# Kernel optimization log

Hardware: AMD Instinct MI355X
Metric: run time of the kernel (lower is better)

The kernel has to match this reference:

```python
import jax, jax.numpy as jnp
import numpy as np

N_NODES = 100000
N_EDGES = 800000
D = 128
N_GRAPHS = 512


def _graph_conv(h, src, dst, norm_src, norm_dst, W, b):
    # DGL GraphConv, norm='both': h' = relu(D_in^{-1/2} * sum_{(u->v)} (D_out^{-1/2} h_u) W + b)
    m = (h * norm_src[:, None])[src]                      # [E, d] gather
    agg = jax.ops.segment_sum(m, dst, num_segments=N_NODES)  # [N, d] scatter-add
    return jax.nn.relu(agg * norm_dst[:, None] @ W + b)


def setup_inputs() -> dict:
    key = jax.random.key(0)
    ks = jax.random.split(key, 10)
    src = jax.random.randint(ks[0], (N_EDGES,), 0, N_NODES)
    dst = jax.random.randint(ks[1], (N_EDGES,), 0, N_NODES)
    graph_ids = jnp.sort(jax.random.randint(ks[2], (N_ODES := N_NODES,), 0, N_GRAPHS))
    features = jax.random.normal(ks[3], (N_NODES, D), dtype=jnp.float32)
    s = 1.0 / np.sqrt(D)
    w1 = jax.random.uniform(ks[4], (D, D), jnp.float32, -s, s)
    b1 = jnp.zeros((D,), jnp.float32)
    w2 = jax.random.uniform(ks[5], (D, D), jnp.float32, -s, s)
    b2 = jnp.zeros((D,), jnp.float32)
    wg = jax.random.uniform(ks[6], (D, 1), jnp.float32, -s, s)
    bg = jnp.zeros((1,), jnp.float32)
    return {"src": src, "dst": dst, "graph_ids": graph_ids, "features": features,
            "w1": w1, "b1": b1, "w2": w2, "b2": b2, "wg": wg, "bg": bg}


def reference(src, dst, graph_ids, features, w1, b1, w2, b2, wg, bg):
    ones = jnp.ones((N_EDGES,), jnp.float32)
    deg_out = jax.ops.segment_sum(ones, src, num_segments=N_NODES)
    deg_in = jax.ops.segment_sum(ones, dst, num_segments=N_NODES)
    norm_src = jax.lax.rsqrt(jnp.maximum(deg_out, 1.0))
    norm_dst = jax.lax.rsqrt(jnp.maximum(deg_in, 1.0))

    h = _graph_conv(features, src, dst, norm_src, norm_dst, w1, b1)
    # dropout is identity in eval mode
    h = _graph_conv(h, src, dst, norm_src, norm_dst, w2, b2)

    # weighted graph aggregation: sigmoid gate per node, per-graph weighted sum
    gate = jax.nn.sigmoid(h @ wg + bg)                    # [N, 1]
    wh = jax.ops.segment_sum(gate * h, graph_ids, num_segments=N_GRAPHS)  # [G, d]
    return wh, h
```

## Files before the change

kernel.cpp:

```cpp
#include <hip/hip_runtime.h>

#define D 128
#define G_GRAPHS 512
#define CCHUNK 4
#define NSLICE 64
#define BINMAX 25088

typedef _Float16 f16;
typedef _Float16 f16x2 __attribute__((ext_vector_type(2)));
typedef _Float16 f16x4 __attribute__((ext_vector_type(4)));
typedef _Float16 f16x8 __attribute__((ext_vector_type(8)));
typedef float f32x2 __attribute__((ext_vector_type(2)));
typedef float f32x4 __attribute__((ext_vector_type(4)));
typedef unsigned short u16;
typedef unsigned char u8;

#define SCAN_CHUNK 2048

__global__ __launch_bounds__(256) void hist_kernel(const int* __restrict__ src, const int* __restrict__ dst,
                                                   u8* __restrict__ pho, u8* __restrict__ phi,
                                                   u8* __restrict__ rank,
                                                   int E, int N, int slice_len, int binsz) {
    __shared__ unsigned hp[(BINMAX + 3) / 4];
    int c = blockIdx.x, role = blockIdx.y, s = blockIdx.z;
    int c0 = c * binsz;
    int lim = min(binsz, N - c0);
    int nw = (lim + 3) >> 2;
    for (int i = threadIdx.x; i < nw; i += 256) hp[i] = 0;
    __syncthreads();
    const int* arr = role ? dst : src;
    int e1 = min(E, (s + 1) * slice_len);
    if (role) {
        for (int e = s * slice_len + (int)threadIdx.x; e < e1; e += 256) {
            unsigned v = (unsigned)(arr[e] - c0);
            if (v < (unsigned)lim) {
                int sh = (v & 3) * 8;
                unsigned old = atomicAdd(&hp[v >> 2], 1u << sh);
                rank[e] = (u8)((old >> sh) & 0xffu);
            }
        }
    } else {
        for (int e = s * slice_len + (int)threadIdx.x; e < e1; e += 256) {
            unsigned v = (unsigned)(arr[e] - c0);
            if (v < (unsigned)lim)
                atomicAdd(&hp[v >> 2], 1u << ((v & 3) * 8));
        }
    }
    __syncthreads();
    u8* outp = (role ? phi : pho) + (size_t)s * N + c0;
    int nw4 = lim >> 2;
    unsigned* o32 = (unsigned*)outp;
    for (int i = threadIdx.x; i < nw4; i += 256) o32[i] = hp[i];
    for (int i = nw4 * 4 + (int)threadIdx.x; i < lim; i += 256)
        outp[i] = (u8)((hp[i >> 2] >> ((i & 3) * 8)) & 0xffu);
}

__global__ __launch_bounds__(256) void merge_prescale_kernel(const u8* __restrict__ pho, u8* __restrict__ phi,
                                                             const float* __restrict__ feat,
                                                             float* __restrict__ norm_src, float* __restrict__ norm_dst,
                                                             int* __restrict__ deg_in_total,
                                                             unsigned* __restrict__ X1,
                                                             const int* __restrict__ gid, int* __restrict__ gstart,
                                                             int mb, int N, int G) {
    if ((int)blockIdx.x >= mb) {
        int n = ((int)blockIdx.x - mb) * 256 + (int)threadIdx.x;
        if (n >= N) return;
        int g = gid[n];
        if (n == 0) {
            for (int x = 0; x <= g; ++x) gstart[x] = 0;
        } else {
            int pg = gid[n - 1];
            for (int x = pg + 1; x <= g; ++x) gstart[x] = n;
        }
        if (n == N - 1) {
            for (int x = g + 1; x <= G; ++x) gstart[x] = N;
        }
        return;
    }
    __shared__ int sumo[4][64];
    __shared__ int sumi[4][64];
    __shared__ float ns_l[64];
    int nl = threadIdx.x & 63;
    int sg = threadIdx.x >> 6;
    int nbase = blockIdx.x * 64;
    int n = nbase + nl;
    int ph_vals[16];
    int po = 0, pp = 0;
    if (n < N) {
        #pragma unroll
        for (int j = 0; j < 16; ++j) {
            int s = sg * 16 + j;
            po += pho[(size_t)s * N + n];
            int v = phi[(size_t)s * N + n];
            ph_vals[j] = v;
            pp += v;
        }
    }
    sumo[sg][nl] = po;
    sumi[sg][nl] = pp;
    __syncthreads();
    if (n < N) {
        int base_i = 0;
        #pragma unroll
        for (int g = 0; g < 4; ++g) base_i += (g < sg) ? sumi[g][nl] : 0;
        int run = base_i;
        #pragma unroll
        for (int j = 0; j < 16; ++j) {
            int s = sg * 16 + j;
            phi[(size_t)s * N + n] = (u8)run;
            run += ph_vals[j];
        }
        if (sg == 0) {
            int tot_o = sumo[0][nl] + sumo[1][nl] + sumo[2][nl] + sumo[3][nl];
            int tot_i = sumi[0][nl] + sumi[1][nl] + sumi[2][nl] + sumi[3][nl];
            float nsv = rsqrtf(fmaxf((float)tot_o, 1.0f));
            norm_src[n] = nsv;
            ns_l[nl] = nsv;
            deg_in_total[n] = tot_i;
            norm_dst[n] = rsqrtf(fmaxf((float)tot_i, 1.0f));
        }
    }
    __syncthreads();
    int cnt = (min(64, N - nbase)) * 32;
    const float4* f4 = (const float4*)feat + (size_t)nbase * 32;
    unsigned* o4 = X1 + (size_t)nbase * 32;
    for (int k = threadIdx.x; k < cnt; k += 256) {
        float4 v = f4[k];
        float s = ns_l[k >> 5];
        int pk = __builtin_amdgcn_cvt_pk_fp8_f32(v.x * s, v.y * s, 0, false);
        pk = __builtin_amdgcn_cvt_pk_fp8_f32(v.z * s, v.w * s, pk, true);
        o4[k] = (unsigned)pk;
    }
}

__global__ __launch_bounds__(256) void scan1_kernel(const int* __restrict__ deg,
                                                    int* __restrict__ partial,
                                                    int* __restrict__ blocksums, int n) {
    __shared__ int wsum[4];
    int lane = threadIdx.x & 63, wid = threadIdx.x >> 6;
    int base = blockIdx.x * SCAN_CHUNK + (int)threadIdx.x * 8;
    int v[8]; int tsum = 0;
    #pragma unroll
    for (int i = 0; i < 8; ++i) { v[i] = (base + i < n) ? deg[base + i] : 0; tsum += v[i]; }
    int s = tsum;
    #pragma unroll
    for (int off = 1; off < 64; off <<= 1) {
        int t = __shfl_up(s, off);
        if (lane >= off) s += t;
    }
    if (lane == 63) wsum[wid] = s;
    __syncthreads();
    int woff = 0;
    for (int w = 0; w < wid; ++w) woff += wsum[w];
    int run = woff + s - tsum;
    #pragma unroll
    for (int i = 0; i < 8; ++i) {
        if (base + i < n) partial[base + i] = run;
        run += v[i];
        if (base + i == n - 1) partial[n] = run;
    }
    if (threadIdx.x == 255) blocksums[blockIdx.x] = woff + s;
}

__global__ void scan2_kernel(int* __restrict__ bs, int nb) {
    int lane = threadIdx.x;
    int carry = 0;
    for (int base = 0; base < nb; base += 64) {
        int i = base + lane;
        int v = (i < nb) ? bs[i] : 0;
        int s = v;
        #pragma unroll
        for (int off = 1; off < 64; off <<= 1) {
            int t = __shfl_up(s, off);
            if (lane >= off) s += t;
        }
        if (i < nb) bs[i] = carry + s - v;
        carry += __shfl(s, 63);
    }
}

__global__ __launch_bounds__(256) void fill_kernel(const int* __restrict__ src, const int* __restrict__ dst,
                                                   const int* __restrict__ partial, const int* __restrict__ bs,
                                                   const u8* __restrict__ phi, const u8* __restrict__ rank,
                                                   int* __restrict__ csr_src,
                                                   int E, int N, int slice_len) {
    int s = blockIdx.y;
    int e = s * slice_len + blockIdx.x * 256 + threadIdx.x;
    int e1 = min(E, (s + 1) * slice_len);
    if (e >= e1) return;
    int d = dst[e];
    int p = partial[d] + bs[d >> 11] + (int)phi[(size_t)s * N + d] + (int)rank[e];
    csr_src[p] = src[e];
}

#define GATHER_BLOCKS 2048
__global__ __launch_bounds__(256) void gather_kernel(const unsigned* __restrict__ x,
                                                     const float* __restrict__ norm_dst,
                                                     const int* __restrict__ partial, const int* __restrict__ bs,
                                                     const int* __restrict__ csr_src,
                                                     f16* __restrict__ A, int N) {
    int wid0 = blockIdx.x * 4 + ((int)threadIdx.x >> 6);
    int lane = threadIdx.x & 63;
    int g = lane >> 4;
    int l = lane & 15;
    for (int node0 = wid0; node0 < N; node0 += GATHER_BLOCKS * 4) {
        int node = __builtin_amdgcn_readfirstlane(node0);
        int beg = partial[node] + bs[node >> 11];
        int end = partial[node + 1] + bs[(node + 1) >> 11];
        float acc0[8] = {0.f}, acc1[8] = {0.f};
        int e = beg;
        for (; e + 8 <= end; e += 8) {
            int sa = csr_src[e + g];
            int sb = csr_src[e + 4 + g];
            uint2 wa = *(const uint2*)(x + (size_t)sa * 32 + l * 2);
            uint2 wb = *(const uint2*)(x + (size_t)sb * 32 + l * 2);
            f32x2 p0 = __builtin_amdgcn_cvt_pk_f32_fp8((int)wa.x, false);
            f32x2 p1 = __builtin_amdgcn_cvt_pk_f32_fp8((int)wa.x, true);
            f32x2 p2 = __builtin_amdgcn_cvt_pk_f32_fp8((int)wa.y, false);
            f32x2 p3 = __builtin_amdgcn_cvt_pk_f32_fp8((int)wa.y, true);
            acc0[0] += p0.x; acc0[1] += p0.y; acc0[2] += p1.x; acc0[3] += p1.y;
            acc0[4] += p2.x; acc0[5] += p2.y; acc0[6] += p3.x; acc0[7] += p3.y;
            f32x2 q0 = __builtin_amdgcn_cvt_pk_f32_fp8((int)wb.x, false);
            f32x2 q1 = __builtin_amdgcn_cvt_pk_f32_fp8((int)wb.x, true);
            f32x2 q2 = __builtin_amdgcn_cvt_pk_f32_fp8((int)wb.y, false);
            f32x2 q3 = __builtin_amdgcn_cvt_pk_f32_fp8((int)wb.y, true);
            acc1[0] += q0.x; acc1[1] += q0.y; acc1[2] += q1.x; acc1[3] += q1.y;
            acc1[4] += q2.x; acc1[5] += q2.y; acc1[6] += q3.x; acc1[7] += q3.y;
        }
        if (e + 4 <= end) {
            int sa = csr_src[e + g];
            uint2 wa = *(const uint2*)(x + (size_t)sa * 32 + l * 2);
            f32x2 p0 = __builtin_amdgcn_cvt_pk_f32_fp8((int)wa.x, false);
            f32x2 p1 = __builtin_amdgcn_cvt_pk_f32_fp8((int)wa.x, true);
            f32x2 p2 = __builtin_amdgcn_cvt_pk_f32_fp8((int)wa.y, false);
            f32x2 p3 = __builtin_amdgcn_cvt_pk_f32_fp8((int)wa.y, true);
            acc0[0] += p0.x; acc0[1] += p0.y; acc0[2] += p1.x; acc0[3] += p1.y;
            acc0[4] += p2.x; acc0[5] += p2.y; acc0[6] += p3.x; acc0[7] += p3.y;
            e += 4;
        }
        int rem = end - e;
        if (g < rem) {
            int sa = csr_src[e + g];
            uint2 wa = *(const uint2*)(x + (size_t)sa * 32 + l * 2);
            f32x2 p0 = __builtin_amdgcn_cvt_pk_f32_fp8((int)wa.x, false);
            f32x2 p1 = __builtin_amdgcn_cvt_pk_f32_fp8((int)wa.x, true);
            f32x2 p2 = __builtin_amdgcn_cvt_pk_f32_fp8((int)wa.y, false);
            f32x2 p3 = __builtin_amdgcn_cvt_pk_f32_fp8((int)wa.y, true);
            acc1[0] += p0.x; acc1[1] += p0.y; acc1[2] += p1.x; acc1[3] += p1.y;
            acc1[4] += p2.x; acc1[5] += p2.y; acc1[6] += p3.x; acc1[7] += p3.y;
        }
        float nd = norm_dst[node];
        f16x8 o;
        #pragma unroll
        for (int j = 0; j < 8; ++j) {
            float v = acc0[j] + acc1[j];
            v += __shfl_xor(v, 16);
            v += __shfl_xor(v, 32);
            o[j] = (f16)(v * nd);
        }
        if (g == 0) *(f16x8*)(A + (size_t)node * D + l * 8) = o;
    }
}

template <typename OutT, bool FP8OUT, bool SCALE, bool GATE>
__global__ __launch_bounds__(256) void gemm_kernel(const f16* __restrict__ A,
                                                   const float* __restrict__ Wg,
                                                   const float* __restrict__ bias,
                                                   const float* __restrict__ rowscale,
                                                   const float* __restrict__ wgv,
                                                   const float* __restrict__ bgv,
                                                   float* __restrict__ gate_out,
                                                   OutT* __restrict__ out, int M) {
    __shared__ f16 Wf[4 * 8 * 64 * 8];
    for (int i = threadIdx.x; i < 2048; i += 256) {
        int kg = i >> 7, j = i & 127;
        int k0 = kg * 8;
        f16x8 tmp;
        #pragma unroll
        for (int b = 0; b < 8; ++b) tmp[b] = (f16)Wg[(k0 + b) * D + j];
        int t = k0 >> 5, c = j >> 4;
        int l = ((k0 & 31) >> 3) * 16 + (j & 15);
        *(f16x8*)&Wf[((t * 8 + c) * 64 + l) * 8] = tmp;
    }
    __syncthreads();
    int wave = threadIdx.x >> 6, lane = threadIdx.x & 63;

    for (int row0 = (blockIdx.x * 4 + wave) * 16; row0 < M; row0 += gridDim.x * 64) {
        int arow = row0 + (lane & 15);
        const f16* Abase = A + arow * D + (lane >> 4) * 8;
        f16x8 a[4];
        #pragma unroll
        for (int t = 0; t < 4; ++t) a[t] = *(const f16x8*)(Abase + t * 32);

        float ns[4];
        if (SCALE) {
            #pragma unroll
            for (int r = 0; r < 4; ++r) ns[r] = rowscale[row0 + (lane >> 4) * 4 + r];
        }
        float dotr[4] = {0.f, 0.f, 0.f, 0.f};

        #pragma unroll
        for (int c = 0; c < 8; ++c) {
            f32x4 acc = {0.f, 0.f, 0.f, 0.f};
            #pragma unroll
            for (int t = 0; t < 4; ++t) {
                f16x8 bf = *(const f16x8*)&Wf[((t * 8 + c) * 64 + lane) * 8];
                acc = __builtin_amdgcn_mfma_f32_16x16x32_f16(a[t], bf, acc, 0, 0, 0);
            }
            int col = c * 16 + (lane & 15);
            float bj = bias[col];
            float wgc = GATE ? wgv[col] : 0.f;
            #pragma unroll
            for (int r = 0; r < 4; ++r) {
                int row = row0 + (lane >> 4) * 4 + r;
                float v = fmaxf(acc[r] + bj, 0.f);
                if (SCALE) v *= ns[r];
                if (FP8OUT) {
                    int pk = __builtin_amdgcn_cvt_pk_fp8_f32(v, v, 0, false);
                    ((u8*)out)[(size_t)row * D + col] = (u8)(pk & 0xff);
                } else {
                    out[(size_t)row * D + col] = (OutT)v;
                }
                if (GATE) dotr[r] += v * wgc;
            }
        }
        if (GATE) {
            float bg0 = bgv[0];
            #pragma unroll
            for (int r = 0; r < 4; ++r) {
                float d = dotr[r];
                d += __shfl_xor(d, 1); d += __shfl_xor(d, 2);
                d += __shfl_xor(d, 4); d += __shfl_xor(d, 8);
                if ((lane & 15) == 0)
                    gate_out[row0 + (lane >> 4) * 4 + r] = 1.0f / (1.0f + __expf(-(d + bg0)));
            }
        }
    }
}

__global__ __launch_bounds__(256) void gagg_kernel(const float* __restrict__ h,
                                                   const float* __restrict__ gate,
                                                   const int* __restrict__ gstart,
                                                   float* __restrict__ wh) {
    __shared__ float part[4][D];
    int g = blockIdx.x;
    int wave = threadIdx.x >> 6, lane = threadIdx.x & 63;
    int beg = gstart[g], end = gstart[g + 1];
    float2 acc = {0.f, 0.f};
    for (int n = beg + wave; n < end; n += 4) {
        float gv = gate[n];
        float2 hv = ((const float2*)(h + n * D))[lane];
        acc.x += gv * hv.x;
        acc.y += gv * hv.y;
    }
    part[wave][lane * 2]     = acc.x;
    part[wave][lane * 2 + 1] = acc.y;
    __syncthreads();
    if (wave == 0) {
        float sx = 0.f, sy = 0.f;
        #pragma unroll
        for (int w = 0; w < 4; ++w) { sx += part[w][lane * 2]; sy += part[w][lane * 2 + 1]; }
        float2 o = {sx, sy};
        ((float2*)(wh + g * D))[lane] = o;
    }
}

extern "C" void kernel_launch(void* const* d_in, const int* in_sizes, int n_in,
                              void* d_out, int out_size, void* d_ws, size_t ws_size,
                              hipStream_t stream) {
    const int*   src  = (const int*)d_in[0];
    const int*   dst  = (const int*)d_in[1];
    const int*   gid  = (const int*)d_in[2];
    const float* feat = (const float*)d_in[3];
    const float* w1   = (const float*)d_in[4];
    const float* b1   = (const float*)d_in[5];
    const float* w2   = (const float*)d_in[6];
    const float* b2   = (const float*)d_in[7];
    const float* wg   = (const float*)d_in[8];
    const float* bg   = (const float*)d_in[9];
    int E = in_sizes[0];
    int N = in_sizes[2];
    const int G = G_GRAPHS;

    int binsz     = (N + CCHUNK - 1) / CCHUNK;
    int slice_len = (E + NSLICE - 1) / NSLICE;
    int bps       = (slice_len + 255) / 256;

    char* ws = (char*)d_ws;
    size_t off = 0;
    auto carve = [&](size_t bytes) { void* p = ws + off; off = (off + bytes + 255) & ~(size_t)255; return p; };
    u8*       pho       = (u8*)      carve((size_t)NSLICE * N);
    u8*       phi       = (u8*)      carve((size_t)NSLICE * N);
    u8*       rank      = (u8*)      carve((size_t)E);
    float*    norm_src  = (float*)   carve((size_t)N * 4);
    float*    norm_dst  = (float*)   carve((size_t)N * 4);
    int*      deg_in_t  = (int*)     carve((size_t)N * 4);
    int*      partial   = (int*)     carve((size_t)(N + 1) * 4);
    int*      blocksums = (int*)     carve((size_t)64 * 4);
    int*      csr_src   = (int*)     carve((size_t)E * 4);
    unsigned* X1        = (unsigned*)carve((size_t)N * D);
    unsigned* X2        = (unsigned*)carve((size_t)N * D);
    f16*      A         = (f16*)     carve((size_t)N * D * 2);
    float*    gate      = (float*)   carve((size_t)N * 4);
    int*      gstart    = (int*)     carve((size_t)(G + 1) * 4);

    float* wh_out = (float*)d_out;
    float* h_out  = (float*)d_out + (size_t)G * D;

    int nb = (N + SCAN_CHUNK - 1) / SCAN_CHUNK;
    int mb = (N + 63) / 64;
    int gb = (N + 255) / 256;

    dim3 hgrid(CCHUNK, 2, NSLICE);
    hist_kernel<<<hgrid, 256, 0, stream>>>(src, dst, pho, phi, rank, E, N, slice_len, binsz);
    merge_prescale_kernel<<<mb + gb, 256, 0, stream>>>(pho, phi, feat, norm_src, norm_dst,
                                                       deg_in_t, X1, gid, gstart, mb, N, G);

    scan1_kernel<<<nb, 256, 0, stream>>>(deg_in_t, partial, blocksums, N);
    scan2_kernel<<<1, 64, 0, stream>>>(blocksums, nb);
    dim3 fgrid(bps, NSLICE);
    fill_kernel<<<fgrid, 256, 0, stream>>>(src, dst, partial, blocksums, phi, rank, csr_src, E, N, slice_len);

    gather_kernel<<<GATHER_BLOCKS, 256, 0, stream>>>(X1, norm_dst, partial, blocksums, csr_src, A, N);
    gemm_kernel<u8, true, true, false><<<256, 256, 0, stream>>>(A, w1, b1, norm_src, nullptr, nullptr, nullptr,
                                                                (u8*)X2, N);
    gather_kernel<<<GATHER_BLOCKS, 256, 0, stream>>>(X2, norm_dst, partial, blocksums, csr_src, A, N);
    gemm_kernel<float, false, false, true><<<256, 256, 0, stream>>>(A, w2, b2, nullptr, wg, bg, gate, h_out, N);

    gagg_kernel<<<G, 256, 0, stream>>>(h_out, gate, gstart, wh_out);
}
```

Measured before the change: 182.3 us.

## Store aggregated features as FP8, fuse scan passes, double histogram slices

The gather kernel now writes its normalized aggregate as packed FP8 instead of f16. The GEMM dequantizes it on load, which halves the traffic through the intermediate A buffer. The separate block-sum scan kernel is removed: a last-block ticket with an atomic counter lets the final scan1 block do the carry scan, saving one launch. NSLICE goes from 64 to 128, giving the histogram and fill kernels more parallelism at the cost of larger per-slice count arrays and more merge work. FP8 storage of the aggregate adds precision loss before the matmul.

```diff
diff --git a/kernel.cpp b/kernel.cpp
--- a/kernel.cpp
+++ b/kernel.cpp
@@ -3,7 +3,7 @@
 #define D 128
 #define G_GRAPHS 512
 #define CCHUNK 4
-#define NSLICE 64
+#define NSLICE 128
 #define BINMAX 25088
 
 typedef _Float16 f16;
@@ -16,6 +16,17 @@
 typedef unsigned char u8;
 
 #define SCAN_CHUNK 2048
+
+__device__ __forceinline__ f16x8 dq8(uint2 w) {
+    f32x2 p0 = __builtin_amdgcn_cvt_pk_f32_fp8((int)w.x, false);
+    f32x2 p1 = __builtin_amdgcn_cvt_pk_f32_fp8((int)w.x, true);
+    f32x2 p2 = __builtin_amdgcn_cvt_pk_f32_fp8((int)w.y, false);
+    f32x2 p3 = __builtin_amdgcn_cvt_pk_f32_fp8((int)w.y, true);
+    f16x8 r;
+    r[0] = (f16)p0.x; r[1] = (f16)p0.y; r[2] = (f16)p1.x; r[3] = (f16)p1.y;
+    r[4] = (f16)p2.x; r[5] = (f16)p2.y; r[6] = (f16)p3.x; r[7] = (f16)p3.y;
+    return r;
+}
 
 __global__ __launch_bounds__(256) void hist_kernel(const int* __restrict__ src, const int* __restrict__ dst,
                                                    u8* __restrict__ pho, u8* __restrict__ phi,
@@ -61,7 +72,9 @@
                                                              int* __restrict__ deg_in_total,
                                                              unsigned* __restrict__ X1,
                                                              const int* __restrict__ gid, int* __restrict__ gstart,
+                                                             int* __restrict__ ticket,
                                                              int mb, int N, int G) {
+    if (blockIdx.x == 0 && threadIdx.x == 0) *ticket = 0;
     if ((int)blockIdx.x >= mb) {
         int n = ((int)blockIdx.x - mb) * 256 + (int)threadIdx.x;
         if (n >= N) return;
@@ -84,12 +97,12 @@
     int sg = threadIdx.x >> 6;
     int nbase = blockIdx.x * 64;
     int n = nbase + nl;
-    int ph_vals[16];
+    int ph_vals[32];
     int po = 0, pp = 0;
     if (n < N) {
-        #pragma unroll
-        for (int j = 0; j < 16; ++j) {
-            int s = sg * 16 + j;
+        #pragma unroll 8
+        for (int j = 0; j < 32; ++j) {
+            int s = sg * 32 + j;
             po += pho[(size_t)s * N + n];
             int v = phi[(size_t)s * N + n];
             ph_vals[j] = v;
@@ -104,9 +117,9 @@
         #pragma unroll
         for (int g = 0; g < 4; ++g) base_i += (g < sg) ? sumi[g][nl] : 0;
         int run = base_i;
-        #pragma unroll
-        for (int j = 0; j < 16; ++j) {
-            int s = sg * 16 + j;
+        #pragma unroll 8
+        for (int j = 0; j < 32; ++j) {
+            int s = sg * 32 + j;
             phi[(size_t)s * N + n] = (u8)run;
             run += ph_vals[j];
         }
@@ -135,8 +148,10 @@
 
 __global__ __launch_bounds__(256) void scan1_kernel(const int* __restrict__ deg,
                                                     int* __restrict__ partial,
-                                                    int* __restrict__ blocksums, int n) {
+                                                    int* __restrict__ blocksums,
+                                                    int* __restrict__ ticket, int n, int nb) {
     __shared__ int wsum[4];
+    __shared__ int lastflag;
     int lane = threadIdx.x & 63, wid = threadIdx.x >> 6;
     int base = blockIdx.x * SCAN_CHUNK + (int)threadIdx.x * 8;
     int v[8]; int tsum = 0;
@@ -159,23 +174,27 @@
         run += v[i];
         if (base + i == n - 1) partial[n] = run;
     }
-    if (threadIdx.x == 255) blocksums[blockIdx.x] = woff + s;
-}
-
-__global__ void scan2_kernel(int* __restrict__ bs, int nb) {
-    int lane = threadIdx.x;
-    int carry = 0;
-    for (int base = 0; base < nb; base += 64) {
-        int i = base + lane;
-        int v = (i < nb) ? bs[i] : 0;
-        int s = v;
-        #pragma unroll
-        for (int off = 1; off < 64; off <<= 1) {
-            int t = __shfl_up(s, off);
-            if (lane >= off) s += t;
-        }
-        if (i < nb) bs[i] = carry + s - v;
-        carry += __shfl(s, 63);
+    if (threadIdx.x == 255) {
+        __hip_atomic_store(&blocksums[blockIdx.x], woff + s, __ATOMIC_RELEASE, __HIP_MEMORY_SCOPE_AGENT);
+        int old = __hip_atomic_fetch_add(ticket, 1, __ATOMIC_ACQ_REL, __HIP_MEMORY_SCOPE_AGENT);
+        lastflag = (old == (int)gridDim.x - 1);
+    }
+    __syncthreads();
+    if (lastflag && threadIdx.x < 64) {
+        int l = threadIdx.x;
+        int carry = 0;
+        for (int b0 = 0; b0 < nb; b0 += 64) {
+            int i = b0 + l;
+            int bv = (i < nb) ? __hip_atomic_load(&blocksums[i], __ATOMIC_ACQUIRE, __HIP_MEMORY_SCOPE_AGENT) : 0;
+            int ss = bv;
+            #pragma unroll
+            for (int off = 1; off < 64; off <<= 1) {
+                int t = __shfl_up(ss, off);
+                if (l >= off) ss += t;
+            }
+            if (i < nb) blocksums[i] = carry + ss - bv;
+            carry += __shfl(ss, 63);
+        }
     }
 }
 
@@ -198,7 +217,7 @@
                                                      const float* __restrict__ norm_dst,
                                                      const int* __restrict__ partial, const int* __restrict__ bs,
                                                      const int* __restrict__ csr_src,
-                                                     f16* __restrict__ A, int N) {
+                                                     unsigned* __restrict__ A, int N) {
     int wid0 = blockIdx.x * 4 + ((int)threadIdx.x >> 6);
     int lane = threadIdx.x & 63;
     int g = lane >> 4;
@@ -250,20 +269,27 @@
             acc1[4] += p2.x; acc1[5] += p2.y; acc1[6] += p3.x; acc1[7] += p3.y;
         }
         float nd = norm_dst[node];
-        f16x8 o;
+        float vv[8];
         #pragma unroll
         for (int j = 0; j < 8; ++j) {
             float v = acc0[j] + acc1[j];
             v += __shfl_xor(v, 16);
             v += __shfl_xor(v, 32);
-            o[j] = (f16)(v * nd);
-        }
-        if (g == 0) *(f16x8*)(A + (size_t)node * D + l * 8) = o;
+            vv[j] = v * nd;
+        }
+        if (g == 0) {
+            int pk0 = __builtin_amdgcn_cvt_pk_fp8_f32(vv[0], vv[1], 0, false);
+            pk0 = __builtin_amdgcn_cvt_pk_fp8_f32(vv[2], vv[3], pk0, true);
+            int pk1 = __builtin_amdgcn_cvt_pk_fp8_f32(vv[4], vv[5], 0, false);
+            pk1 = __builtin_amdgcn_cvt_pk_fp8_f32(vv[6], vv[7], pk1, true);
+            uint2 o; o.x = (unsigned)pk0; o.y = (unsigned)pk1;
+            *(uint2*)(A + (size_t)node * 32 + l * 2) = o;
+        }
     }
 }
 
 template <typename OutT, bool FP8OUT, bool SCALE, bool GATE>
-__global__ __launch_bounds__(256) void gemm_kernel(const f16* __restrict__ A,
+__global__ __launch_bounds__(256) void gemm_kernel(const unsigned* __restrict__ A8,
                                                    const float* __restrict__ Wg,
                                                    const float* __restrict__ bias,
                                                    const float* __restrict__ rowscale,
@@ -284,13 +310,14 @@
     }
     __syncthreads();
     int wave = threadIdx.x >> 6, lane = threadIdx.x & 63;
+    const uint2* A2 = (const uint2*)A8;
 
     for (int row0 = (blockIdx.x * 4 + wave) * 16; row0 < M; row0 += gridDim.x * 64) {
         int arow = row0 + (lane & 15);
-        const f16* Abase = A + arow * D + (lane >> 4) * 8;
         f16x8 a[4];
         #pragma unroll
-        for (int t = 0; t < 4; ++t) a[t] = *(const f16x8*)(Abase + t * 32);
+        for (int t = 0; t < 4; ++t)
+            a[t] = dq8(A2[(size_t)arow * 16 + t * 4 + (lane >> 4)]);
 
         float ns[4];
         if (SCALE) {
@@ -397,10 +424,11 @@
     int*      deg_in_t  = (int*)     carve((size_t)N * 4);
     int*      partial   = (int*)     carve((size_t)(N + 1) * 4);
     int*      blocksums = (int*)     carve((size_t)64 * 4);
+    int*      ticket    = (int*)     carve((size_t)256);
     int*      csr_src   = (int*)     carve((size_t)E * 4);
     unsigned* X1        = (unsigned*)carve((size_t)N * D);
     unsigned* X2        = (unsigned*)carve((size_t)N * D);
-    f16*      A         = (f16*)     carve((size_t)N * D * 2);
+    unsigned* A         = (unsigned*)carve((size_t)N * D);
     float*    gate      = (float*)   carve((size_t)N * 4);
     int*      gstart    = (int*)     carve((size_t)(G + 1) * 4);
 
@@ -414,10 +442,9 @@
     dim3 hgrid(CCHUNK, 2, NSLICE);
     hist_kernel<<<hgrid, 256, 0, stream>>>(src, dst, pho, phi, rank, E, N, slice_len, binsz);
     merge_prescale_kernel<<<mb + gb, 256, 0, stream>>>(pho, phi, feat, norm_src, norm_dst,
-                                                       deg_in_t, X1, gid, gstart, mb, N, G);
-
-    scan1_kernel<<<nb, 256, 0, stream>>>(deg_in_t, partial, blocksums, N);
-    scan2_kernel<<<1, 64, 0, stream>>>(blocksums, nb);
+                                                       deg_in_t, X1, gid, gstart, ticket, mb, N, G);
+
+    scan1_kernel<<<nb, 256, 0, stream>>>(deg_in_t, partial, blocksums, ticket, N, nb);
     dim3 fgrid(bps, NSLICE);
     fill_kernel<<<fgrid, 256, 0, stream>>>(src, dst, partial, blocksums, phi, rank, csr_src, E, N, slice_len);
 
```

New measurement: 183.9 us. Within noise of the previous version (+0.9%).
